# Optimization experiments

Measured on AMD Instinct MI355X. Metric: run time of the kernel, lower is better.

The kernel has to match this reference:

```python
import jax, jax.numpy as jnp
import numpy as np

B, S, D, H = 2, 2048, 1024, 16
DK = D // H


def setup_inputs() -> dict:
    key = jax.random.key(0)
    ks = jax.random.split(key, 13)
    scale = 1.0 / np.sqrt(D)
    return {
        "query": jax.random.normal(ks[0], (B, S, D), jnp.float32),
        "key": jax.random.normal(ks[1], (B, S, D), jnp.float32),
        "value": jax.random.normal(ks[2], (B, S, D), jnp.float32),
        "mask": jax.random.randint(ks[3], (B, S, S), 0, 2, jnp.int32),
        "Wq": jax.random.normal(ks[4], (D, D), jnp.float32) * scale,
        "bq": jnp.zeros((D,), jnp.float32),
        "Wk": jax.random.normal(ks[5], (D, D), jnp.float32) * scale,
        "bk": jnp.zeros((D,), jnp.float32),
        "Wv": jax.random.normal(ks[6], (D, D), jnp.float32) * scale,
        "bv": jnp.zeros((D,), jnp.float32),
        "Wo": jax.random.normal(ks[7], (D, D), jnp.float32) * scale,
        "bo": jnp.zeros((D,), jnp.float32),
    }


def _split_heads(x):
    # [B,S,D] -> [B,H,S,DK]
    b, s, _ = x.shape
    return x.reshape(b, s, H, DK).transpose(0, 2, 1, 3)


def reference(query, key, value, mask, Wq, bq, Wk, bk, Wv, bv, Wo, bo):
    q = _split_heads(query @ Wq + bq)
    k = _split_heads(key @ Wk + bk)
    v = _split_heads(value @ Wv + bv)
    # scaled dot-product scores [B,H,Sq,Sk]
    scores = jnp.einsum("bhqd,bhkd->bhqk", q, k) / jnp.sqrt(jnp.float32(DK))
    scores = jnp.where(mask[:, None, :, :] == 0, jnp.float32(-1e9), scores)
    p_attn = jax.nn.softmax(scores, axis=-1)  # dropout p=0.0 -> identity
    x = jnp.einsum("bhqk,bhkd->bhqd", p_attn, v)
    x = x.transpose(0, 2, 1, 3).reshape(query.shape[0], -1, D)
    return x @ Wo + bo
```

## Files before the change

kernel.cpp:

```cpp
#include <hip/hip_runtime.h>
#include <cstdint>

#define B_ 2
#define S_ 2048
#define D_ 1024
#define H_ 16
#define DK_ 64
#define SCALE_ 0.18033688011112042f

typedef float f32x4 __attribute__((ext_vector_type(4)));
typedef float f32x16 __attribute__((ext_vector_type(16)));
typedef __bf16 bf16x8 __attribute__((ext_vector_type(8)));
typedef unsigned short u16x8 __attribute__((ext_vector_type(8)));
typedef unsigned short u16x4 __attribute__((ext_vector_type(4)));
typedef unsigned int u32x4 __attribute__((ext_vector_type(4)));

__device__ __forceinline__ unsigned short f2bf(float x) {
  unsigned int u = __builtin_bit_cast(unsigned int, x);
  u += 0x7FFFu + ((u >> 16) & 1u);
  return (unsigned short)(u >> 16);
}

__device__ __forceinline__ void gload16(const void* g, void* l) {
  __builtin_amdgcn_global_load_lds((__attribute__((address_space(1))) void*)(void*)g,
                                   (__attribute__((address_space(3))) void*)l, 16, 0, 0);
}

__device__ __forceinline__ float exp2v(float x) {
  float r;
  asm("v_exp_f32 %0, %1" : "=v"(r) : "v"(x));
  return r;
}

__device__ __forceinline__ unsigned int cvtpk(float a, float b) {
  unsigned int r;
  asm("v_cvt_pk_bf16_f32 %0, %1, %2" : "=v"(r) : "v"(a), "v"(b));
  return r;
}

__device__ __forceinline__ unsigned int bit_mask(unsigned int w, int bit) {
#if __has_builtin(__builtin_amdgcn_sbfe)
  return (unsigned int)__builtin_amdgcn_sbfe((int)w, bit, 1);
#else
  return (unsigned int)((int)(w << (31 - bit)) >> 31);
#endif
}

__global__ __launch_bounds__(256) void prep_kernel(
    const float* __restrict__ q, const float* __restrict__ k, const float* __restrict__ v,
    unsigned short* __restrict__ oq, unsigned short* __restrict__ ok,
    unsigned short* __restrict__ ov,
    const float* __restrict__ w0, const float* __restrict__ w1,
    const float* __restrict__ w2, const float* __restrict__ w3,
    unsigned short* o0, unsigned short* o1, unsigned short* o2, unsigned short* o3,
    const int* __restrict__ mask, unsigned int* __restrict__ mb) {
  __shared__ float t[32][33];
  const int bid = blockIdx.x;
  const int tid = threadIdx.x;
  if (bid < 6144) {
    const int z = bid >> 11, vb = bid & 2047;
    const float* in = z == 0 ? q : z == 1 ? k : v;
    unsigned short* out = z == 0 ? oq : z == 1 ? ok : ov;
    const int n = B_ * S_ * D_;
    int idx = vb * 256 + tid;
#pragma unroll
    for (int i = idx * 4; i < n; i += 2048 * 256 * 4) {
      f32x4 vv = *(const f32x4*)(in + i);
      u16x4 o;
#pragma unroll
      for (int j = 0; j < 4; ++j) o[j] = f2bf(vv[j]);
      *(u16x4*)(out + i) = o;
    }
  } else if (bid < 10240) {
    const int r = bid - 6144;
    const int z = r >> 10, rr = r & 1023;
    const float* W;
    unsigned short* O;
    float sc = 1.f;
    if (z == 0) { W = w0; O = o0; sc = SCALE_; }
    else if (z == 1) { W = w1; O = o1; }
    else if (z == 2) { W = w2; O = o2; }
    else { W = w3; O = o3; }
    const int n0 = (rr & 31) * 32, k0 = (rr >> 5) * 32;
    const int tx = tid & 31, ty = tid >> 5;
    for (int i = ty; i < 32; i += 8) t[i][tx] = W[(size_t)(k0 + i) * D_ + n0 + tx];
    __syncthreads();
    for (int i = ty; i < 32; i += 8) O[(size_t)(n0 + i) * D_ + k0 + tx] = f2bf(t[tx][i] * sc);
  } else {
    const int wid = ((bid - 10240) << 2) + (tid >> 6);
    const int lane = tid & 63;
    size_t base = (size_t)wid << 6;
    unsigned long long bits = __ballot(mask[base + lane] != 0);
    if (lane == 0) *(unsigned long long*)(mb + (base >> 5)) = bits;
  }
}

template <int MODE, int TN, int NWN>
__device__ __forceinline__ void gemm_t(const unsigned short* __restrict__ A,
                                       const unsigned short* __restrict__ BT,
                                       const float* __restrict__ bias, float bsc,
                                       void* __restrict__ Cp, int M, int N, int K) {
  constexpr int NWM = 4 / NWN;
  constexpr int WM = 128 / NWM;
  constexpr int WN = TN / NWN;
  constexpr int MR = WM / 16, NR = WN / 16;
  __shared__ unsigned short Al[2][128 * 32];
  __shared__ unsigned short Bl[2][TN * 32];
  const int tid = threadIdx.x;
  const int lane = tid & 63;
  const int w = tid >> 6;
  const int wr = w / NWN, wc = w % NWN;
  const int nwg = gridDim.x * gridDim.y;
  const int wg = blockIdx.x + gridDim.x * blockIdx.y;
  const int work = (wg & 7) * (nwg >> 3) + (wg >> 3);
  const int nx = N / TN;
  const int m0 = (work / nx) * 128, n0 = (work % nx) * TN;

  f32x4 acc[MR][NR] = {};
  const int nk = K / 32;
  const int srow = lane >> 2;
  const int scol = ((lane & 3) ^ ((lane >> 3) & 3)) * 8;

  const int fr = lane & 15;
  const int rsw = ((lane >> 4) ^ ((fr >> 1) & 3)) * 8;

  auto stage = [&](int kt, int bufi) {
#pragma unroll
    for (int it = 0; it < 2; ++it) {
      int chunk = it * 4 + w;
      gload16(A + (size_t)(m0 + chunk * 16 + srow) * K + kt * 32 + scol,
              &Al[bufi][chunk * 512]);
    }
#pragma unroll
    for (int it = 0; it < TN / 64; ++it) {
      int chunk = it * 4 + w;
      gload16(BT + (size_t)(n0 + chunk * 16 + srow) * K + kt * 32 + scol,
              &Bl[bufi][chunk * 512]);
    }
  };

  stage(0, 0);
  for (int kt = 0; kt < nk; ++kt) {
    const int buf = kt & 1;
    __syncthreads();
    if (kt + 1 < nk) stage(kt + 1, buf ^ 1);
    bf16x8 af[MR], bf[NR];
#pragma unroll
    for (int i = 0; i < MR; ++i)
      af[i] = __builtin_bit_cast(bf16x8,
          *(const u16x8*)&Al[buf][(wr * WM + i * 16 + fr) * 32 + rsw]);
#pragma unroll
    for (int j = 0; j < NR; ++j)
      bf[j] = __builtin_bit_cast(bf16x8,
          *(const u16x8*)&Bl[buf][(wc * WN + j * 16 + fr) * 32 + rsw]);
    __builtin_amdgcn_s_setprio(1);
#pragma unroll
    for (int i = 0; i < MR; ++i)
#pragma unroll
      for (int j = 0; j < NR; ++j)
        acc[i][j] = __builtin_amdgcn_mfma_f32_16x16x32_bf16(af[i], bf[j], acc[i][j], 0, 0, 0);
    __builtin_amdgcn_s_setprio(0);
  }

  const int rg = (lane >> 4) * 4;
  const int cg = lane & 15;
#pragma unroll
  for (int i = 0; i < MR; ++i)
#pragma unroll
    for (int j = 0; j < NR; ++j) {
      int col = n0 + wc * WN + j * 16 + cg;
      float bv = bias[col] * bsc;
#pragma unroll
      for (int e = 0; e < 4; ++e) {
        int row = m0 + wr * WM + i * 16 + rg + e;
        float v = acc[i][j][e] + bv;
        if (MODE == 1)
          ((float*)Cp)[(size_t)row * N + col] = v;
        else if (MODE == 0)
          ((unsigned short*)Cp)[(size_t)row * N + col] = f2bf(v);
        else
          ((unsigned short*)Cp)[((size_t)(row >> 11) * D_ + col) * S_ + (row & (S_ - 1))] = f2bf(v);
      }
    }
}

__global__ __launch_bounds__(256) void qkv_gemm_kernel(
    const unsigned short* __restrict__ xq, const unsigned short* __restrict__ xk,
    const unsigned short* __restrict__ xv, const unsigned short* __restrict__ wtq,
    const unsigned short* __restrict__ wtk, const unsigned short* __restrict__ wtv,
    const float* __restrict__ bq, const float* __restrict__ bk, const float* __restrict__ bv,
    unsigned short* q, unsigned short* k, unsigned short* vt) {
  if (blockIdx.z == 0)
    gemm_t<0, 128, 2>(xq, wtq, bq, SCALE_, (void*)q, B_ * S_, D_, D_);
  else if (blockIdx.z == 1)
    gemm_t<0, 128, 2>(xk, wtk, bk, 1.f, (void*)k, B_ * S_, D_, D_);
  else
    gemm_t<2, 128, 2>(xv, wtv, bv, 1.f, (void*)vt, B_ * S_, D_, D_);
}

__global__ __launch_bounds__(256) void out_gemm_kernel(const unsigned short* __restrict__ x,
                                                       const unsigned short* __restrict__ wto,
                                                       const float* __restrict__ bo,
                                                       float* __restrict__ out) {
  gemm_t<1, 64, 1>(x, wto, bo, 1.f, (void*)out, B_ * S_, D_, D_);
}

__global__ __launch_bounds__(256, 2) void attn_kernel(const unsigned short* __restrict__ Q,
                                                      const unsigned short* __restrict__ K,
                                                      const unsigned short* __restrict__ Vt,
                                                      const unsigned int* __restrict__ mb,
                                                      unsigned short* __restrict__ X) {
  __shared__ unsigned short Kl[2][128 * 64];
  __shared__ unsigned short Vl[2][2][64 * 64];

  const int tid = threadIdx.x;
  const int lane = tid & 63;
  const int w = tid >> 6;
  const int ql = lane & 31;
  const int hi = lane >> 5;

  const int wg = blockIdx.x + gridDim.x * blockIdx.y;
  const int swz = (wg & 7) * 64 + (wg >> 3);
  const int qt = swz & 15;
  const int bh = swz >> 4;
  const int b = bh >> 4, h = bh & 15;
  const int q_g = qt * 128 + w * 32 + ql;

  const size_t qkbase = ((size_t)b * S_) * D_ + h * DK_;
  const size_t vtbase = ((size_t)b * D_ + h * DK_) * S_;

  bf16x8 qf[4];
  {
    const unsigned short* qp = Q + qkbase + (size_t)q_g * D_ + hi * 8;
#pragma unroll
    for (int c = 0; c < 4; ++c)
      qf[c] = __builtin_bit_cast(bf16x8, *(const u16x8*)(qp + c * 16));
  }

  const int lr = lane >> 3;
  const int seg = (lane & 7) ^ lr;
  const unsigned short* Ks = K + qkbase + (size_t)(w * 32 + lr) * D_ + seg * 8;
  const unsigned short* Vs = Vt + vtbase + (size_t)(w * 16 + lr) * S_ + seg * 8;

  auto stage = [&](int kt, int bufi) {
#pragma unroll
    for (int c = 0; c < 4; ++c)
      gload16(Ks + ((size_t)kt * 128 + c * 8) * D_, &Kl[bufi][(w * 32 + c * 8) * 64]);
#pragma unroll
    for (int c = 0; c < 4; ++c)
      gload16(Vs + (size_t)((c & 1) * 8) * S_ + kt * 128 + (c >> 1) * 64,
              &Vl[bufi][c >> 1][(w * 16 + (c & 1) * 8) * 64]);
  };

  const unsigned long long* mrow =
      (const unsigned long long*)mb + ((size_t)b * S_ + q_g) * 32;

  f32x16 o0 = {}, o1 = {};
  f32x16 o2 = {};
  const int sw = (ql & 7) << 4;

  const unsigned int one2 = 0x3F803F80u;
  const bf16x8 onesf = __builtin_bit_cast(bf16x8, u32x4{one2, one2, one2, one2});

  stage(0, 0);
  const int NT = S_ / 128;
  unsigned long long M0n = mrow[0], M1n = mrow[1];

  for (int kt = 0; kt < NT; ++kt) {
    const int buf = kt & 1;
    __syncthreads();
    unsigned long long M0 = M0n, M1 = M1n;

    bf16x8 kf[2][2][4];
#pragma unroll
    for (int hh = 0; hh < 2; ++hh) {
      const char* Kb = (const char*)&Kl[buf][hh * 64 * 64];
#pragma unroll
      for (int r = 0; r < 2; ++r)
#pragma unroll
        for (int c = 0; c < 4; ++c)
          kf[hh][r][c] = __builtin_bit_cast(
              bf16x8, *(const u16x8*)(Kb + (((r * 32 + ql) * 128 + c * 32 + hi * 16) ^ sw)));
    }
    if (kt < NT - 1) {
      stage(kt + 1, buf ^ 1);
      M0n = mrow[kt * 2 + 2];
      M1n = mrow[kt * 2 + 3];
    }

    f32x16 s[2][2] = {};
    __builtin_amdgcn_s_setprio(1);
#pragma unroll
    for (int hh = 0; hh < 2; ++hh)
#pragma unroll
      for (int c = 0; c < 4; ++c) {
        s[hh][0] = __builtin_amdgcn_mfma_f32_32x32x16_bf16(kf[hh][0][c], qf[c], s[hh][0], 0, 0, 0);
        s[hh][1] = __builtin_amdgcn_mfma_f32_32x32x16_bf16(kf[hh][1][c], qf[c], s[hh][1], 0, 0, 0);
      }
    __builtin_amdgcn_s_setprio(0);

    bf16x8 vf[2][2][4];
#pragma unroll
    for (int hh = 0; hh < 2; ++hh) {
      const char* Vb = (const char*)&Vl[buf][hh][0];
#pragma unroll
      for (int nt = 0; nt < 2; ++nt)
#pragma unroll
        for (int kc = 0; kc < 4; ++kc)
          vf[hh][nt][kc] = __builtin_bit_cast(
              bf16x8, *(const u16x8*)(Vb + (((nt * 32 + ql) * 128 + kc * 32 + hi * 16) ^ sw)));
    }

    u32x4 pw[2][4];
#pragma unroll
    for (int hh = 0; hh < 2; ++hh) {
      const unsigned long long M = hh ? M1 : M0;
      unsigned int W0 = (unsigned int)(M >> (hi * 4));
      unsigned int W1 = (unsigned int)(M >> (32 + hi * 4));
#pragma unroll
      for (int r = 0; r < 16; ++r) {
        const int krl = (r & 3) + 8 * (r >> 2);
        unsigned int mk0 = bit_mask(W0, krl);
        float p0 = exp2v(s[hh][0][r]);
        s[hh][0][r] = __builtin_bit_cast(float, __builtin_bit_cast(unsigned int, p0) & mk0);
        unsigned int mk1 = bit_mask(W1, krl);
        float p1 = exp2v(s[hh][1][r]);
        s[hh][1][r] = __builtin_bit_cast(float, __builtin_bit_cast(unsigned int, p1) & mk1);
      }
#pragma unroll
      for (int kc = 0; kc < 4; ++kc) {
        const int rb = (kc & 1) * 8;
        const int st = kc >> 1;
        unsigned int w0 = cvtpk(s[hh][st][rb + 0], s[hh][st][rb + 1]);
        unsigned int w1 = cvtpk(s[hh][st][rb + 2], s[hh][st][rb + 3]);
        unsigned int w2 = cvtpk(s[hh][st][rb + 4], s[hh][st][rb + 5]);
        unsigned int w3 = cvtpk(s[hh][st][rb + 6], s[hh][st][rb + 7]);
        unsigned int u0, u1, u2, u3;
#if __has_builtin(__builtin_amdgcn_permlane32_swap)
        { auto r02 = __builtin_amdgcn_permlane32_swap(w0, w2, false, false);
          u0 = r02[0]; u2 = r02[1]; }
        { auto r13 = __builtin_amdgcn_permlane32_swap(w1, w3, false, false);
          u1 = r13[0]; u3 = r13[1]; }
#else
        { unsigned int t0 = (unsigned int)__shfl_xor((int)w0, 32);
          unsigned int t2 = (unsigned int)__shfl_xor((int)w2, 32);
          u0 = hi ? t2 : w0; u2 = hi ? w2 : t0;
          unsigned int t1 = (unsigned int)__shfl_xor((int)w1, 32);
          unsigned int t3 = (unsigned int)__shfl_xor((int)w3, 32);
          u1 = hi ? t3 : w1; u3 = hi ? w3 : t1; }
#endif
        pw[hh][kc] = u32x4{u0, u1, u2, u3};
      }
    }

    __builtin_amdgcn_s_setprio(1);
#pragma unroll
    for (int hh = 0; hh < 2; ++hh)
#pragma unroll
      for (int kc = 0; kc < 4; ++kc) {
        bf16x8 pf = __builtin_bit_cast(bf16x8, pw[hh][kc]);
        o0 = __builtin_amdgcn_mfma_f32_32x32x16_bf16(vf[hh][0][kc], pf, o0, 0, 0, 0);
        o1 = __builtin_amdgcn_mfma_f32_32x32x16_bf16(vf[hh][1][kc], pf, o1, 0, 0, 0);
        o2 = __builtin_amdgcn_mfma_f32_32x32x16_bf16(onesf, pf, o2, 0, 0, 0);
      }
    __builtin_amdgcn_s_setprio(0);
  }

  float inv = 1.f / o2[0];
  unsigned short* Xp = X + ((size_t)b * S_ + q_g) * D_ + h * DK_;
#pragma unroll
  for (int rb = 0; rb < 4; ++rb) {
    int d0 = 8 * rb + 4 * hi;
    *(unsigned int*)(Xp + d0) = cvtpk(o0[4 * rb + 0] * inv, o0[4 * rb + 1] * inv);
    *(unsigned int*)(Xp + d0 + 2) = cvtpk(o0[4 * rb + 2] * inv, o0[4 * rb + 3] * inv);
    *(unsigned int*)(Xp + 32 + d0) = cvtpk(o1[4 * rb + 0] * inv, o1[4 * rb + 1] * inv);
    *(unsigned int*)(Xp + 32 + d0 + 2) = cvtpk(o1[4 * rb + 2] * inv, o1[4 * rb + 3] * inv);
  }
}

extern "C" void kernel_launch(void* const* d_in, const int* in_sizes, int n_in,
                              void* d_out, int out_size, void* d_ws, size_t ws_size,
                              hipStream_t stream) {
  const float* query = (const float*)d_in[0];
  const float* key = (const float*)d_in[1];
  const float* value = (const float*)d_in[2];
  const int* mask = (const int*)d_in[3];
  const float* Wq = (const float*)d_in[4];
  const float* bq = (const float*)d_in[5];
  const float* Wk = (const float*)d_in[6];
  const float* bk = (const float*)d_in[7];
  const float* Wv = (const float*)d_in[8];
  const float* bv = (const float*)d_in[9];
  const float* Wo = (const float*)d_in[10];
  const float* bo = (const float*)d_in[11];
  float* out = (float*)d_out;

  const size_t ACT = (size_t)B_ * S_ * D_;
  const size_t WSZ = (size_t)D_ * D_;
  unsigned short* ws = (unsigned short*)d_ws;
  unsigned short* xq = ws;
  unsigned short* xk = xq + ACT;
  unsigned short* xv = xk + ACT;
  unsigned short* wtq = xv + ACT;
  unsigned short* wtk = wtq + WSZ;
  unsigned short* wtv = wtk + WSZ;
  unsigned short* wto = wtv + WSZ;
  unsigned short* qb = wto + WSZ;
  unsigned short* kb = qb + ACT;
  unsigned short* vt = kb + ACT;
  unsigned int* mbp = (unsigned int*)(vt + ACT);
  unsigned short* xb = xq;

  prep_kernel<<<43008, 256, 0, stream>>>(query, key, value, xq, xk, xv,
                                         Wq, Wk, Wv, Wo, wtq, wtk, wtv, wto,
                                         mask, mbp);

  dim3 gg(8, 32, 3);
  qkv_gemm_kernel<<<gg, 256, 0, stream>>>(xq, xk, xv, wtq, wtk, wtv, bq, bk, bv, qb, kb, vt);

  dim3 ag(S_ / 128, B_ * H_);
  attn_kernel<<<ag, 256, 0, stream>>>(qb, kb, vt, mbp, xb);

  dim3 og(16, 32, 1);
  out_gemm_kernel<<<og, 256, 0, stream>>>(xb, wto, bo, out);
}
```

Measured before the change: 154.4 us.

## Fuse fp32-to-bf16 activation conversion into QKV GEMM A-tile staging

Drops the separate pass that converted query, key and value from fp32 to bf16 in the prep kernel. The QKV GEMM now reads fp32 A tiles straight into registers, packs them to bf16 with v_cvt_pk_bf16_f32, and writes them to swizzled LDS after the MFMA block, prefetching one K-tile ahead. This removes one write and one read of three activation tensors in bf16 and shrinks the prep launch. In exchange the GEMM reads twice as many A bytes, and A staging now goes through registers instead of direct global-to-LDS loads, which raises register pressure.

```diff
diff --git a/kernel.cpp b/kernel.cpp
--- a/kernel.cpp
+++ b/kernel.cpp
@@ -47,9 +47,6 @@
 }
 
 __global__ __launch_bounds__(256) void prep_kernel(
-    const float* __restrict__ q, const float* __restrict__ k, const float* __restrict__ v,
-    unsigned short* __restrict__ oq, unsigned short* __restrict__ ok,
-    unsigned short* __restrict__ ov,
     const float* __restrict__ w0, const float* __restrict__ w1,
     const float* __restrict__ w2, const float* __restrict__ w3,
     unsigned short* o0, unsigned short* o1, unsigned short* o2, unsigned short* o3,
@@ -57,23 +54,8 @@
   __shared__ float t[32][33];
   const int bid = blockIdx.x;
   const int tid = threadIdx.x;
-  if (bid < 6144) {
-    const int z = bid >> 11, vb = bid & 2047;
-    const float* in = z == 0 ? q : z == 1 ? k : v;
-    unsigned short* out = z == 0 ? oq : z == 1 ? ok : ov;
-    const int n = B_ * S_ * D_;
-    int idx = vb * 256 + tid;
-#pragma unroll
-    for (int i = idx * 4; i < n; i += 2048 * 256 * 4) {
-      f32x4 vv = *(const f32x4*)(in + i);
-      u16x4 o;
-#pragma unroll
-      for (int j = 0; j < 4; ++j) o[j] = f2bf(vv[j]);
-      *(u16x4*)(out + i) = o;
-    }
-  } else if (bid < 10240) {
-    const int r = bid - 6144;
-    const int z = r >> 10, rr = r & 1023;
+  if (bid < 4096) {
+    const int z = bid >> 10, rr = bid & 1023;
     const float* W;
     unsigned short* O;
     float sc = 1.f;
@@ -87,7 +69,7 @@
     __syncthreads();
     for (int i = ty; i < 32; i += 8) O[(size_t)(n0 + i) * D_ + k0 + tx] = f2bf(t[tx][i] * sc);
   } else {
-    const int wid = ((bid - 10240) << 2) + (tid >> 6);
+    const int wid = ((bid - 4096) << 2) + (tid >> 6);
     const int lane = tid & 63;
     size_t base = (size_t)wid << 6;
     unsigned long long bits = __ballot(mask[base + lane] != 0);
@@ -95,8 +77,8 @@
   }
 }
 
-template <int MODE, int TN, int NWN>
-__device__ __forceinline__ void gemm_t(const unsigned short* __restrict__ A,
+template <int MODE, int TN, int NWN, bool AF32>
+__device__ __forceinline__ void gemm_t(const void* __restrict__ Ap,
                                        const unsigned short* __restrict__ BT,
                                        const float* __restrict__ bias, float bsc,
                                        void* __restrict__ Cp, int M, int N, int K) {
@@ -106,6 +88,8 @@
   constexpr int MR = WM / 16, NR = WN / 16;
   __shared__ unsigned short Al[2][128 * 32];
   __shared__ unsigned short Bl[2][TN * 32];
+  const unsigned short* A16 = (const unsigned short*)Ap;
+  const float* A32 = (const float*)Ap;
   const int tid = threadIdx.x;
   const int lane = tid & 63;
   const int w = tid >> 6;
@@ -119,31 +103,68 @@
   f32x4 acc[MR][NR] = {};
   const int nk = K / 32;
   const int srow = lane >> 2;
-  const int scol = ((lane & 3) ^ ((lane >> 3) & 3)) * 8;
+  const int sxor = ((lane & 3) ^ ((srow >> 1) & 3)) * 8;
+  const int scol_lin = (lane & 3) * 8;
 
   const int fr = lane & 15;
   const int rsw = ((lane >> 4) ^ ((fr >> 1) & 3)) * 8;
 
-  auto stage = [&](int kt, int bufi) {
+  auto stageB = [&](int kt, int bufi) {
+#pragma unroll
+    for (int it = 0; it < TN / 64; ++it) {
+      int chunk = it * 4 + w;
+      gload16(BT + (size_t)(n0 + chunk * 16 + srow) * K + kt * 32 + sxor,
+              &Bl[bufi][chunk * 512]);
+    }
+  };
+  auto stageA16 = [&](int kt, int bufi) {
 #pragma unroll
     for (int it = 0; it < 2; ++it) {
       int chunk = it * 4 + w;
-      gload16(A + (size_t)(m0 + chunk * 16 + srow) * K + kt * 32 + scol,
+      gload16(A16 + (size_t)(m0 + chunk * 16 + srow) * K + kt * 32 + sxor,
               &Al[bufi][chunk * 512]);
     }
-#pragma unroll
-    for (int it = 0; it < TN / 64; ++it) {
+  };
+
+  f32x4 aR[2][2];
+  auto loadA32 = [&](int kt) {
+#pragma unroll
+    for (int it = 0; it < 2; ++it) {
       int chunk = it * 4 + w;
-      gload16(BT + (size_t)(n0 + chunk * 16 + srow) * K + kt * 32 + scol,
-              &Bl[bufi][chunk * 512]);
+      const float* ga = A32 + (size_t)(m0 + chunk * 16 + srow) * K + kt * 32 + scol_lin;
+      aR[it][0] = *(const f32x4*)ga;
+      aR[it][1] = *(const f32x4*)(ga + 4);
     }
   };
-
-  stage(0, 0);
+  auto writeA = [&](int bufi) {
+#pragma unroll
+    for (int it = 0; it < 2; ++it) {
+      int chunk = it * 4 + w;
+      u32x4 pk;
+      pk[0] = cvtpk(aR[it][0][0], aR[it][0][1]);
+      pk[1] = cvtpk(aR[it][0][2], aR[it][0][3]);
+      pk[2] = cvtpk(aR[it][1][0], aR[it][1][1]);
+      pk[3] = cvtpk(aR[it][1][2], aR[it][1][3]);
+      *(u32x4*)&Al[bufi][chunk * 512 + srow * 32 + sxor] = pk;
+    }
+  };
+
+  if (AF32) {
+    loadA32(0);
+    writeA(0);
+    if (nk > 1) loadA32(1);
+  } else {
+    stageA16(0, 0);
+  }
+  stageB(0, 0);
+
   for (int kt = 0; kt < nk; ++kt) {
     const int buf = kt & 1;
     __syncthreads();
-    if (kt + 1 < nk) stage(kt + 1, buf ^ 1);
+    if (kt + 1 < nk) {
+      stageB(kt + 1, buf ^ 1);
+      if (!AF32) stageA16(kt + 1, buf ^ 1);
+    }
     bf16x8 af[MR], bf[NR];
 #pragma unroll
     for (int i = 0; i < MR; ++i)
@@ -160,6 +181,10 @@
       for (int j = 0; j < NR; ++j)
         acc[i][j] = __builtin_amdgcn_mfma_f32_16x16x32_bf16(af[i], bf[j], acc[i][j], 0, 0, 0);
     __builtin_amdgcn_s_setprio(0);
+    if (AF32 && kt + 1 < nk) {
+      writeA(buf ^ 1);
+      if (kt + 2 < nk) loadA32(kt + 2);
+    }
   }
 
   const int rg = (lane >> 4) * 4;
@@ -185,24 +210,24 @@
 }
 
 __global__ __launch_bounds__(256) void qkv_gemm_kernel(
-    const unsigned short* __restrict__ xq, const unsigned short* __restrict__ xk,
-    const unsigned short* __restrict__ xv, const unsigned short* __restrict__ wtq,
+    const float* __restrict__ query, const float* __restrict__ key,
+    const float* __restrict__ value, const unsigned short* __restrict__ wtq,
     const unsigned short* __restrict__ wtk, const unsigned short* __restrict__ wtv,
     const float* __restrict__ bq, const float* __restrict__ bk, const float* __restrict__ bv,
     unsigned short* q, unsigned short* k, unsigned short* vt) {
   if (blockIdx.z == 0)
-    gemm_t<0, 128, 2>(xq, wtq, bq, SCALE_, (void*)q, B_ * S_, D_, D_);
+    gemm_t<0, 128, 2, true>(query, wtq, bq, SCALE_, (void*)q, B_ * S_, D_, D_);
   else if (blockIdx.z == 1)
-    gemm_t<0, 128, 2>(xk, wtk, bk, 1.f, (void*)k, B_ * S_, D_, D_);
+    gemm_t<0, 128, 2, true>(key, wtk, bk, 1.f, (void*)k, B_ * S_, D_, D_);
   else
-    gemm_t<2, 128, 2>(xv, wtv, bv, 1.f, (void*)vt, B_ * S_, D_, D_);
+    gemm_t<2, 128, 2, true>(value, wtv, bv, 1.f, (void*)vt, B_ * S_, D_, D_);
 }
 
 __global__ __launch_bounds__(256) void out_gemm_kernel(const unsigned short* __restrict__ x,
                                                        const unsigned short* __restrict__ wto,
                                                        const float* __restrict__ bo,
                                                        float* __restrict__ out) {
-  gemm_t<1, 64, 1>(x, wto, bo, 1.f, (void*)out, B_ * S_, D_, D_);
+  gemm_t<1, 64, 1, false>(x, wto, bo, 1.f, (void*)out, B_ * S_, D_, D_);
 }
 
 __global__ __launch_bounds__(256, 2) void attn_kernel(const unsigned short* __restrict__ Q,
@@ -398,10 +423,7 @@
   const size_t ACT = (size_t)B_ * S_ * D_;
   const size_t WSZ = (size_t)D_ * D_;
   unsigned short* ws = (unsigned short*)d_ws;
-  unsigned short* xq = ws;
-  unsigned short* xk = xq + ACT;
-  unsigned short* xv = xk + ACT;
-  unsigned short* wtq = xv + ACT;
+  unsigned short* wtq = ws;
   unsigned short* wtk = wtq + WSZ;
   unsigned short* wtv = wtk + WSZ;
   unsigned short* wto = wtv + WSZ;
@@ -409,14 +431,13 @@
   unsigned short* kb = qb + ACT;
   unsigned short* vt = kb + ACT;
   unsigned int* mbp = (unsigned int*)(vt + ACT);
-  unsigned short* xb = xq;
-
-  prep_kernel<<<43008, 256, 0, stream>>>(query, key, value, xq, xk, xv,
-                                         Wq, Wk, Wv, Wo, wtq, wtk, wtv, wto,
-                                         mask, mbp);
+  unsigned short* xb = (unsigned short*)(mbp + (size_t)B_ * S_ * S_ / 32);
+
+  prep_kernel<<<36864, 256, 0, stream>>>(Wq, Wk, Wv, Wo, wtq, wtk, wtv, wto, mask, mbp);
 
   dim3 gg(8, 32, 3);
-  qkv_gemm_kernel<<<gg, 256, 0, stream>>>(xq, xk, xv, wtq, wtk, wtv, bq, bk, bv, qb, kb, vt);
+  qkv_gemm_kernel<<<gg, 256, 0, stream>>>(query, key, value, wtq, wtk, wtv,
+                                          bq, bk, bv, qb, kb, vt);
 
   dim3 ag(S_ / 128, B_ * H_);
   attn_kernel<<<ag, 256, 0, stream>>>(qb, kb, vt, mbp, xb);
```

After: 150.6 us. -2.5%, faster.

## Triple-buffer GEMM LDS staging and pack four mask ballots per wave

Applied to the files above, without the earlier changes.

The shared GEMM template now uses a three-stage LDS ring, issuing loads two k-tiles ahead, with explicit vmcnt waits and raw s_barrier instead of __syncthreads. The aim is to hide global-to-LDS latency in the QKV and output projections. The mask bit-packing path now has each wave handle 256 ints with four ballots, which cuts the prep grid from 43008 to 18432 blocks. The deeper pipeline adds LDS use per block and depends on hand-counted waitcnt values being correct; the global-load swizzle column formula was also rewritten.

```diff
diff --git a/kernel.cpp b/kernel.cpp
--- a/kernel.cpp
+++ b/kernel.cpp
@@ -87,25 +87,35 @@
     __syncthreads();
     for (int i = ty; i < 32; i += 8) O[(size_t)(n0 + i) * D_ + k0 + tx] = f2bf(t[tx][i] * sc);
   } else {
-    const int wid = ((bid - 10240) << 2) + (tid >> 6);
-    const int lane = tid & 63;
-    size_t base = (size_t)wid << 6;
-    unsigned long long bits = __ballot(mask[base + lane] != 0);
-    if (lane == 0) *(unsigned long long*)(mb + (base >> 5)) = bits;
+    const int blk = bid - 10240;
+    const int w = tid >> 6, lane = tid & 63;
+    const size_t base = ((size_t)blk * 4 + w) * 256;
+    const int* mp = mask + base;
+    unsigned long long b0 = __ballot(mp[lane] != 0);
+    unsigned long long b1 = __ballot(mp[64 + lane] != 0);
+    unsigned long long b2 = __ballot(mp[128 + lane] != 0);
+    unsigned long long b3 = __ballot(mp[192 + lane] != 0);
+    if (lane == 0) {
+      unsigned long long* dst = (unsigned long long*)(mb + (base >> 5));
+      dst[0] = b0; dst[1] = b1; dst[2] = b2; dst[3] = b3;
+    }
   }
 }
 
-template <int MODE, int TN, int NWN>
-__device__ __forceinline__ void gemm_t(const unsigned short* __restrict__ A,
+template <int MODE, int TM, int TN, int NWM, int NWN>
+__device__ __forceinline__ void gemm_t(const unsigned short* __restrict__ A16,
                                        const unsigned short* __restrict__ BT,
                                        const float* __restrict__ bias, float bsc,
-                                       void* __restrict__ Cp, int M, int N, int K) {
-  constexpr int NWM = 4 / NWN;
-  constexpr int WM = 128 / NWM;
+                                       void* __restrict__ Cp,
+                                       unsigned short* __restrict__ AlS,
+                                       unsigned short* __restrict__ BlS,
+                                       int M, int N, int K) {
+  static_assert(NWM * NWN == 4, "4 waves");
+  constexpr int WM = TM / NWM;
   constexpr int WN = TN / NWN;
   constexpr int MR = WM / 16, NR = WN / 16;
-  __shared__ unsigned short Al[2][128 * 32];
-  __shared__ unsigned short Bl[2][TN * 32];
+  constexpr int ASTRIDE = TM * 32;
+  constexpr int BSTRIDE = TN * 32;
   const int tid = threadIdx.x;
   const int lane = tid & 63;
   const int w = tid >> 6;
@@ -114,45 +124,40 @@
   const int wg = blockIdx.x + gridDim.x * blockIdx.y;
   const int work = (wg & 7) * (nwg >> 3) + (wg >> 3);
   const int nx = N / TN;
-  const int m0 = (work / nx) * 128, n0 = (work % nx) * TN;
+  const int m0 = (work / nx) * TM, n0 = (work % nx) * TN;
 
   f32x4 acc[MR][NR] = {};
   const int nk = K / 32;
   const int srow = lane >> 2;
-  const int scol = ((lane & 3) ^ ((lane >> 3) & 3)) * 8;
+  const int sxor = ((lane & 3) ^ ((srow >> 1) & 3)) * 8;
 
   const int fr = lane & 15;
   const int rsw = ((lane >> 4) ^ ((fr >> 1) & 3)) * 8;
 
   auto stage = [&](int kt, int bufi) {
 #pragma unroll
-    for (int it = 0; it < 2; ++it) {
+    for (int it = 0; it < TM / 64; ++it) {
       int chunk = it * 4 + w;
-      gload16(A + (size_t)(m0 + chunk * 16 + srow) * K + kt * 32 + scol,
-              &Al[bufi][chunk * 512]);
+      gload16(A16 + (size_t)(m0 + chunk * 16 + srow) * K + kt * 32 + sxor,
+              AlS + bufi * ASTRIDE + chunk * 512);
     }
 #pragma unroll
     for (int it = 0; it < TN / 64; ++it) {
       int chunk = it * 4 + w;
-      gload16(BT + (size_t)(n0 + chunk * 16 + srow) * K + kt * 32 + scol,
-              &Bl[bufi][chunk * 512]);
+      gload16(BT + (size_t)(n0 + chunk * 16 + srow) * K + kt * 32 + sxor,
+              BlS + bufi * BSTRIDE + chunk * 512);
     }
   };
-
-  stage(0, 0);
-  for (int kt = 0; kt < nk; ++kt) {
-    const int buf = kt & 1;
-    __syncthreads();
-    if (kt + 1 < nk) stage(kt + 1, buf ^ 1);
+  auto compute = [&](int bufi) {
     bf16x8 af[MR], bf[NR];
 #pragma unroll
     for (int i = 0; i < MR; ++i)
       af[i] = __builtin_bit_cast(bf16x8,
-          *(const u16x8*)&Al[buf][(wr * WM + i * 16 + fr) * 32 + rsw]);
+          *(const u16x8*)(AlS + bufi * ASTRIDE + (wr * WM + i * 16 + fr) * 32 + rsw));
 #pragma unroll
     for (int j = 0; j < NR; ++j)
       bf[j] = __builtin_bit_cast(bf16x8,
-          *(const u16x8*)&Bl[buf][(wc * WN + j * 16 + fr) * 32 + rsw]);
+          *(const u16x8*)(BlS + bufi * BSTRIDE + (wc * WN + j * 16 + fr) * 32 + rsw));
     __builtin_amdgcn_s_setprio(1);
 #pragma unroll
     for (int i = 0; i < MR; ++i)
@@ -160,6 +165,25 @@
       for (int j = 0; j < NR; ++j)
         acc[i][j] = __builtin_amdgcn_mfma_f32_16x16x32_bf16(af[i], bf[j], acc[i][j], 0, 0, 0);
     __builtin_amdgcn_s_setprio(0);
+  };
+
+  constexpr int SLOADS = TM / 64 + TN / 64;
+  stage(0, 0);
+  if (nk > 1) stage(1, 1);
+  asm volatile("s_waitcnt vmcnt(%0) lgkmcnt(0)" :: "i"(SLOADS) : "memory");
+  __builtin_amdgcn_s_barrier();
+  __builtin_amdgcn_sched_barrier(0);
+  for (int kt = 0; kt < nk; ++kt) {
+    if (kt + 2 < nk) stage(kt + 2, (kt + 2) % 3);
+    compute(kt % 3);
+    if (kt + 1 < nk) {
+      if (kt + 2 < nk)
+        asm volatile("s_waitcnt vmcnt(%0) lgkmcnt(0)" :: "i"(SLOADS) : "memory");
+      else
+        asm volatile("s_waitcnt vmcnt(0) lgkmcnt(0)" ::: "memory");
+      __builtin_amdgcn_s_barrier();
+      __builtin_amdgcn_sched_barrier(0);
+    }
   }
 
   const int rg = (lane >> 4) * 4;
@@ -190,19 +214,23 @@
     const unsigned short* __restrict__ wtk, const unsigned short* __restrict__ wtv,
     const float* __restrict__ bq, const float* __restrict__ bk, const float* __restrict__ bv,
     unsigned short* q, unsigned short* k, unsigned short* vt) {
+  __shared__ alignas(16) unsigned short As[3 * 128 * 32];
+  __shared__ alignas(16) unsigned short Bs[3 * 128 * 32];
   if (blockIdx.z == 0)
-    gemm_t<0, 128, 2>(xq, wtq, bq, SCALE_, (void*)q, B_ * S_, D_, D_);
+    gemm_t<0, 128, 128, 2, 2>(xq, wtq, bq, SCALE_, (void*)q, As, Bs, B_ * S_, D_, D_);
   else if (blockIdx.z == 1)
-    gemm_t<0, 128, 2>(xk, wtk, bk, 1.f, (void*)k, B_ * S_, D_, D_);
+    gemm_t<0, 128, 128, 2, 2>(xk, wtk, bk, 1.f, (void*)k, As, Bs, B_ * S_, D_, D_);
   else
-    gemm_t<2, 128, 2>(xv, wtv, bv, 1.f, (void*)vt, B_ * S_, D_, D_);
+    gemm_t<2, 128, 128, 2, 2>(xv, wtv, bv, 1.f, (void*)vt, As, Bs, B_ * S_, D_, D_);
 }
 
 __global__ __launch_bounds__(256) void out_gemm_kernel(const unsigned short* __restrict__ x,
                                                        const unsigned short* __restrict__ wto,
                                                        const float* __restrict__ bo,
                                                        float* __restrict__ out) {
-  gemm_t<1, 64, 1>(x, wto, bo, 1.f, (void*)out, B_ * S_, D_, D_);
+  __shared__ alignas(16) unsigned short As[3 * 128 * 32];
+  __shared__ alignas(16) unsigned short Bs[3 * 64 * 32];
+  gemm_t<1, 128, 64, 4, 1>(x, wto, bo, 1.f, (void*)out, As, Bs, B_ * S_, D_, D_);
 }
 
 __global__ __launch_bounds__(256, 2) void attn_kernel(const unsigned short* __restrict__ Q,
@@ -411,12 +439,13 @@
   unsigned int* mbp = (unsigned int*)(vt + ACT);
   unsigned short* xb = xq;
 
-  prep_kernel<<<43008, 256, 0, stream>>>(query, key, value, xq, xk, xv,
+  prep_kernel<<<18432, 256, 0, stream>>>(query, key, value, xq, xk, xv,
                                          Wq, Wk, Wv, Wo, wtq, wtk, wtv, wto,
                                          mask, mbp);
 
   dim3 gg(8, 32, 3);
-  qkv_gemm_kernel<<<gg, 256, 0, stream>>>(xq, xk, xv, wtq, wtk, wtv, bq, bk, bv, qb, kb, vt);
+  qkv_gemm_kernel<<<gg, 256, 0, stream>>>(xq, xk, xv, wtq, wtk, wtv,
+                                          bq, bk, bv, qb, kb, vt);
 
   dim3 ag(S_ / 128, B_ * H_);
   attn_kernel<<<ag, 256, 0, stream>>>(qb, kb, vt, mbp, xb);
```

Result: faster. 147.3 us (-4.6%).
